# Performance work log

Hardware: AMD Instinct MI355X
Metric: run time of the kernel (lower is better)

The kernel has to match this reference:

```python
import jax, jax.numpy as jnp
import numpy as np

N, E = 50000, 1600000
IN_C, HEADS, OUT_C = 128, 4, 32


def setup_inputs() -> dict:
    key = jax.random.key(0)
    ks = jax.random.split(key, 8)
    x = jax.random.normal(ks[0], (N, IN_C), dtype=jnp.float32)
    row = jnp.sort(jax.random.randint(ks[1], (E,), 0, N, dtype=jnp.int32)).astype(jnp.int64)
    col = jax.random.randint(ks[2], (E,), 0, N, dtype=jnp.int64)
    # xavier_uniform-style params
    def xavier(k, shape, fan_in, fan_out):
        lim = float(np.sqrt(6.0 / (fan_in + fan_out)))
        return jax.random.uniform(k, shape, jnp.float32, -lim, lim)
    weight = xavier(ks[3], (IN_C, HEADS * OUT_C), IN_C, HEADS * OUT_C)
    att_src = xavier(ks[4], (1, HEADS, OUT_C), HEADS, OUT_C)
    att_dst = xavier(ks[5], (1, HEADS, OUT_C), HEADS, OUT_C)
    bias = jnp.zeros((HEADS * OUT_C,), jnp.float32)
    return {"x": x, "weight": weight, "att_src": att_src, "att_dst": att_dst,
            "bias": bias, "row": row, "col": col}


def reference(x, weight, att_src, att_dst, bias, row, col):
    n = x.shape[0]
    H, C = att_src.shape[1], att_src.shape[2]
    xp = (x @ weight).reshape(n, H, C)                 # [N,H,C]
    a_src = jnp.sum(xp * att_src, axis=-1)             # [N,H]
    a_dst = jnp.sum(xp * att_dst, axis=-1)             # [N,H]
    alpha = jax.nn.leaky_relu(a_src[row] + a_dst[col], negative_slope=0.2)  # [E,H]
    # torch scatter_reduce amax with include_self=True over a zeros buffer -> max(0, seg_max)
    amax = jnp.maximum(jax.ops.segment_max(alpha, row, num_segments=n), 0.0)
    alpha = jnp.exp(alpha - amax[row])
    asum = jax.ops.segment_sum(alpha, row, num_segments=n)
    alpha = alpha / (asum[row] + 1e-8)                 # [E,H]
    msg = alpha[:, :, None] * xp[col]                  # [E,H,C]
    out = jax.ops.segment_sum(msg, row, num_segments=n).reshape(n, H * C)
    return out + bias
```

## Files before the change

kernel.cpp:

```cpp
#include <hip/hip_runtime.h>
#include <hip/hip_bf16.h>


#define IN_C 128
#define HC 128
#define STG 256

typedef __attribute__((ext_vector_type(8))) __bf16 bfrag_t;
typedef __attribute__((ext_vector_type(4))) float f32x4;
union frag_u { uint4 u; bfrag_t b; };

static __device__ inline unsigned short f2bf(float f) {
    unsigned u = __float_as_uint(f);
    unsigned r = (u + 0x7fffu + ((u >> 16) & 1u)) >> 16;
    return (unsigned short)r;
}
static __device__ inline unsigned pack2(float a, float b) {
    return (unsigned)f2bf(a) | ((unsigned)f2bf(b) << 16);
}
static __device__ inline float bf_lo(unsigned u) { return __uint_as_float(u << 16); }
static __device__ inline float bf_hi(unsigned u) { return __uint_as_float(u & 0xffff0000u); }

__global__ __launch_bounds__(256) void prep_kernel(const float* __restrict__ W,
                                                   unsigned short* __restrict__ wt,
                                                   const int* __restrict__ row,
                                                   int* __restrict__ row_ptr,
                                                   int n_nodes, int E) {
    int gid = blockIdx.x * 256 + threadIdx.x;
    if (gid < IN_C * HC) {
        int n = gid >> 7, k = gid & 127;
        wt[((size_t)n * 16 + ((k >> 3) ^ (n & 7))) * 8 + (k & 7)] =
            f2bf(W[(size_t)k * HC + n]);
    }
    if (gid < E) {
        int lane = threadIdx.x & 63;
        int r1 = row[gid];
        int r0 = __shfl_up(r1, 1, 64);
        if (lane == 0) r0 = (gid == 0) ? -1 : row[gid - 1];
        for (int v = r0 + 1; v <= r1; ++v) row_ptr[v] = gid;
        if (gid == E - 1)
            for (int v = r1 + 1; v <= n_nodes; ++v) row_ptr[v] = E;
    }
}

__global__ __launch_bounds__(512) void gemm_kernel(const float* __restrict__ x,
                                                   const uint4* __restrict__ wt,
                                                   const float* __restrict__ attS,
                                                   const float* __restrict__ attD,
                                                   unsigned short* __restrict__ xp,
                                                   float* __restrict__ a_src,
                                                   float* __restrict__ a_dst, int n_nodes) {
    __shared__ uint4 Bl[2048];
    __shared__ uint4 Al[2048];
    const int tid = threadIdx.x;
    const int base = blockIdx.x * 128;

    #pragma unroll
    for (int i = 0; i < 4; ++i) Bl[tid + 512 * i] = wt[tid + 512 * i];

    #pragma unroll
    for (int i = 0; i < 4; ++i) {
        int idx = tid + 512 * i;
        int row = idx >> 4, chunk = idx & 15;
        uint4 p = make_uint4(0u, 0u, 0u, 0u);
        if (base + row < n_nodes) {
            const float* src = x + (size_t)(base + row) * IN_C + chunk * 8;
            float4 lo = *(const float4*)src;
            float4 hi = *(const float4*)(src + 4);
            p.x = pack2(lo.x, lo.y); p.y = pack2(lo.z, lo.w);
            p.z = pack2(hi.x, hi.y); p.w = pack2(hi.z, hi.w);
        }
        Al[row * 16 + (chunk ^ (row & 7))] = p;
    }
    __syncthreads();

    const int w = tid >> 6, l = tid & 63, l15 = l & 15, q = l >> 4;
    f32x4 acc[8] = {};
    const int arow = 16 * w + l15;
    #pragma unroll
    for (int ks = 0; ks < 4; ++ks) {
        frag_u a; a.u = Al[arow * 16 + ((ks * 4 + q) ^ (arow & 7))];
        #pragma unroll
        for (int t = 0; t < 8; ++t) {
            int brow = 16 * t + l15;
            frag_u b; b.u = Bl[brow * 16 + ((ks * 4 + q) ^ (brow & 7))];
            acc[t] = __builtin_amdgcn_mfma_f32_16x16x32_bf16(a.b, b.b, acc[t], 0, 0, 0);
        }
    }

    float avS[8], avD[8];
    #pragma unroll
    for (int t = 0; t < 8; ++t) {
        avS[t] = attS[16 * t + l15];
        avD[t] = attD[16 * t + l15];
    }
    float hpS[4][4] = {}, hpD[4][4] = {};
    #pragma unroll
    for (int t = 0; t < 8; ++t) {
        #pragma unroll
        for (int r = 0; r < 4; ++r) {
            float v = acc[t][r];
            hpS[r][t >> 1] = fmaf(v, avS[t], hpS[r][t >> 1]);
            hpD[r][t >> 1] = fmaf(v, avD[t], hpD[r][t >> 1]);
            int grow = base + 16 * w + 4 * q + r;
            if (grow < n_nodes)
                xp[(size_t)grow * HC + 16 * t + l15] = f2bf(v);
        }
    }
    #pragma unroll
    for (int r = 0; r < 4; ++r) {
        #pragma unroll
        for (int h = 0; h < 4; ++h) {
            #pragma unroll
            for (int off = 1; off < 16; off <<= 1) {
                hpS[r][h] += __shfl_xor(hpS[r][h], off, 64);
                hpD[r][h] += __shfl_xor(hpD[r][h], off, 64);
            }
        }
        int grow = base + 16 * w + 4 * q + r;
        if (l15 == 0 && grow < n_nodes) {
            *(float4*)(a_src + (size_t)grow * 4) =
                make_float4(hpS[r][0], hpS[r][1], hpS[r][2], hpS[r][3]);
            *(float4*)(a_dst + (size_t)grow * 4) =
                make_float4(hpD[r][0], hpD[r][1], hpD[r][2], hpD[r][3]);
        }
    }
}

__global__ __launch_bounds__(256, 8) void agg_kernel(const unsigned* __restrict__ xp,
                                                     const float* __restrict__ a_src,
                                                     const float* __restrict__ a_dst,
                                                     const int* __restrict__ col,
                                                     const int* __restrict__ row_ptr,
                                                     const float* __restrict__ bias,
                                                     float* __restrict__ out, int n_nodes) {
    __shared__ uint2 lds_w[4][STG];
    __shared__ int   lds_c[4][STG];
    const int wid = threadIdx.x >> 6, lane = threadIdx.x & 63;
    const int n = blockIdx.x * 4 + wid;
    const bool alive = n < n_nodes;

    int start = 0, deg = 0;
    if (alive) { start = row_ptr[n]; deg = row_ptr[n + 1] - start; }
    const bool staged = deg <= STG;
    float4 as4 = alive ? *(const float4*)(a_src + (size_t)n * 4)
                       : make_float4(0.f, 0.f, 0.f, 0.f);

    float s0 = 0.f, s1 = 0.f, s2 = 0.f, s3 = 0.f;
    for (int i = lane; i < deg; i += 64) {
        int cc = col[start + i];
        float4 ad = *(const float4*)(a_dst + (size_t)cc * 4);
        float v0 = as4.x + ad.x, v1 = as4.y + ad.y, v2 = as4.z + ad.z, v3 = as4.w + ad.w;
        v0 = v0 > 0.f ? v0 : 0.2f * v0;  v1 = v1 > 0.f ? v1 : 0.2f * v1;
        v2 = v2 > 0.f ? v2 : 0.2f * v2;  v3 = v3 > 0.f ? v3 : 0.2f * v3;
        float w0 = __expf(v0), w1 = __expf(v1), w2 = __expf(v2), w3 = __expf(v3);
        if (staged) {
            lds_c[wid][i] = cc;
            lds_w[wid][i] = make_uint2(pack2(w0, w1), pack2(w2, w3));
        }
        s0 += w0; s1 += w1; s2 += w2; s3 += w3;
    }
    #pragma unroll
    for (int off = 1; off < 64; off <<= 1) {
        s0 += __shfl_xor(s0, off, 64);
        s1 += __shfl_xor(s1, off, 64);
        s2 += __shfl_xor(s2, off, 64);
        s3 += __shfl_xor(s3, off, 64);
    }

    const int h = lane >> 4;
    const float sh = h == 0 ? s0 : h == 1 ? s1 : h == 2 ? s2 : s3;
    const float inv = 1.0f / (sh + 1e-8f);
    const unsigned* xpl = xp + lane;
    float ac0 = 0.f, ac1 = 0.f;

    if (staged) {
        const uint2* wr = &lds_w[wid][0];
        const int*   cr = &lds_c[wid][0];
        int i = 0;
        for (; i + 8 <= deg; i += 8) {
            int c0 = cr[i+0], c1 = cr[i+1], c2 = cr[i+2], c3 = cr[i+3];
            int c4 = cr[i+4], c5 = cr[i+5], c6 = cr[i+6], c7 = cr[i+7];
            uint2 q0 = wr[i+0], q1 = wr[i+1], q2 = wr[i+2], q3 = wr[i+3];
            uint2 q4 = wr[i+4], q5 = wr[i+5], q6 = wr[i+6], q7 = wr[i+7];
            unsigned u0 = xpl[(size_t)c0 * 64];
            unsigned u1 = xpl[(size_t)c1 * 64];
            unsigned u2 = xpl[(size_t)c2 * 64];
            unsigned u3 = xpl[(size_t)c3 * 64];
            unsigned u4 = xpl[(size_t)c4 * 64];
            unsigned u5 = xpl[(size_t)c5 * 64];
            unsigned u6 = xpl[(size_t)c6 * 64];
            unsigned u7 = xpl[(size_t)c7 * 64];
            unsigned x0 = (h & 2) ? q0.y : q0.x;
            unsigned x1 = (h & 2) ? q1.y : q1.x;
            unsigned x2 = (h & 2) ? q2.y : q2.x;
            unsigned x3 = (h & 2) ? q3.y : q3.x;
            unsigned x4 = (h & 2) ? q4.y : q4.x;
            unsigned x5 = (h & 2) ? q5.y : q5.x;
            unsigned x6 = (h & 2) ? q6.y : q6.x;
            unsigned x7 = (h & 2) ? q7.y : q7.x;
            float w0 = (h & 1) ? bf_hi(x0) : bf_lo(x0);
            float w1 = (h & 1) ? bf_hi(x1) : bf_lo(x1);
            float w2 = (h & 1) ? bf_hi(x2) : bf_lo(x2);
            float w3 = (h & 1) ? bf_hi(x3) : bf_lo(x3);
            float w4 = (h & 1) ? bf_hi(x4) : bf_lo(x4);
            float w5 = (h & 1) ? bf_hi(x5) : bf_lo(x5);
            float w6 = (h & 1) ? bf_hi(x6) : bf_lo(x6);
            float w7 = (h & 1) ? bf_hi(x7) : bf_lo(x7);
            ac0 = fmaf(w0, bf_lo(u0), ac0);  ac1 = fmaf(w0, bf_hi(u0), ac1);
            ac0 = fmaf(w1, bf_lo(u1), ac0);  ac1 = fmaf(w1, bf_hi(u1), ac1);
            ac0 = fmaf(w2, bf_lo(u2), ac0);  ac1 = fmaf(w2, bf_hi(u2), ac1);
            ac0 = fmaf(w3, bf_lo(u3), ac0);  ac1 = fmaf(w3, bf_hi(u3), ac1);
            ac0 = fmaf(w4, bf_lo(u4), ac0);  ac1 = fmaf(w4, bf_hi(u4), ac1);
            ac0 = fmaf(w5, bf_lo(u5), ac0);  ac1 = fmaf(w5, bf_hi(u5), ac1);
            ac0 = fmaf(w6, bf_lo(u6), ac0);  ac1 = fmaf(w6, bf_hi(u6), ac1);
            ac0 = fmaf(w7, bf_lo(u7), ac0);  ac1 = fmaf(w7, bf_hi(u7), ac1);
        }
        for (; i < deg; ++i) {
            int c0 = cr[i];
            uint2 q0 = wr[i];
            unsigned x0 = (h & 2) ? q0.y : q0.x;
            float w0 = (h & 1) ? bf_hi(x0) : bf_lo(x0);
            unsigned u0 = xpl[(size_t)c0 * 64];
            ac0 = fmaf(w0, bf_lo(u0), ac0);  ac1 = fmaf(w0, bf_hi(u0), ac1);
        }
    } else {
        const float ash = h == 0 ? as4.x : h == 1 ? as4.y : h == 2 ? as4.z : as4.w;
        for (int i = 0; i < deg; ++i) {
            int c0 = col[start + i];
            float v = ash + a_dst[(size_t)c0 * 4 + h];
            v = v > 0.f ? v : 0.2f * v;
            float w0 = __expf(v);
            unsigned u0 = xpl[(size_t)c0 * 64];
            ac0 = fmaf(w0, bf_lo(u0), ac0);  ac1 = fmaf(w0, bf_hi(u0), ac1);
        }
    }

    if (alive) {
        float2 bv = *(const float2*)(bias + 2 * lane);
        *(float2*)(out + (size_t)n * HC + 2 * lane) =
            make_float2(ac0 * inv + bv.x, ac1 * inv + bv.y);
    }
}

extern "C" void kernel_launch(void* const* d_in, const int* in_sizes, int n_in,
                              void* d_out, int out_size, void* d_ws, size_t ws_size,
                              hipStream_t stream) {
    const float* x       = (const float*)d_in[0];
    const float* weight  = (const float*)d_in[1];
    const float* att_src = (const float*)d_in[2];
    const float* att_dst = (const float*)d_in[3];
    const float* bias    = (const float*)d_in[4];
    const int*   row     = (const int*)d_in[5];
    const int*   col     = (const int*)d_in[6];
    float* out = (float*)d_out;

    const int n_nodes = in_sizes[0] / IN_C;
    const int E = in_sizes[5];

    char* ws = (char*)d_ws;
    unsigned short* xp = (unsigned short*)ws;  ws += (size_t)n_nodes * HC * sizeof(unsigned short);
    float* a_src   = (float*)ws;               ws += (size_t)n_nodes * 4 * sizeof(float);
    float* a_dst   = (float*)ws;               ws += (size_t)n_nodes * 4 * sizeof(float);
    unsigned short* wt = (unsigned short*)ws;  ws += (size_t)IN_C * HC * sizeof(unsigned short);
    int*   row_ptr = (int*)ws;                 ws += (size_t)(n_nodes + 1) * sizeof(int);

    prep_kernel<<<(E + 255) / 256, 256, 0, stream>>>(weight, wt, row, row_ptr, n_nodes, E);
    gemm_kernel<<<(n_nodes + 127) / 128, 512, 0, stream>>>(x, (const uint4*)wt,
                                                           att_src, att_dst,
                                                           xp, a_src, a_dst, n_nodes);
    agg_kernel<<<(n_nodes + 3) / 4, 256, 0, stream>>>((const unsigned*)xp, a_src, a_dst,
                                                      col, row_ptr, bias, out, n_nodes);
}
```

Before: 84.32 us.

## Move row_ptr construction into GEMM kernel and stage xp stores through LDS

The CSR row_ptr build moves out of the prep kernel, which now only converts weights with a small grid, and into the GEMM kernel, where each block handles a contiguous slice of edges. The GEMM's bf16 output is first written to shared memory and then stored to global memory as coalesced 16-byte rows, replacing scattered 2-byte stores. This is meant to shorten the large prep launch and improve write coalescing. The cost is extra LDS traffic and barriers in the GEMM, and the GEMM blocks now also do the edge scan.

```diff
diff --git a/kernel.cpp b/kernel.cpp
--- a/kernel.cpp
+++ b/kernel.cpp
@@ -22,55 +22,58 @@
 static __device__ inline float bf_hi(unsigned u) { return __uint_as_float(u & 0xffff0000u); }
 
 __global__ __launch_bounds__(256) void prep_kernel(const float* __restrict__ W,
-                                                   unsigned short* __restrict__ wt,
-                                                   const int* __restrict__ row,
-                                                   int* __restrict__ row_ptr,
-                                                   int n_nodes, int E) {
+                                                   unsigned short* __restrict__ wt) {
     int gid = blockIdx.x * 256 + threadIdx.x;
-    if (gid < IN_C * HC) {
-        int n = gid >> 7, k = gid & 127;
-        wt[((size_t)n * 16 + ((k >> 3) ^ (n & 7))) * 8 + (k & 7)] =
-            f2bf(W[(size_t)k * HC + n]);
-    }
-    if (gid < E) {
-        int lane = threadIdx.x & 63;
-        int r1 = row[gid];
-        int r0 = __shfl_up(r1, 1, 64);
-        if (lane == 0) r0 = (gid == 0) ? -1 : row[gid - 1];
-        for (int v = r0 + 1; v <= r1; ++v) row_ptr[v] = gid;
-        if (gid == E - 1)
-            for (int v = r1 + 1; v <= n_nodes; ++v) row_ptr[v] = E;
-    }
+    int n = gid >> 7, k = gid & 127;
+    wt[((size_t)n * 16 + ((k >> 3) ^ (n & 7))) * 8 + (k & 7)] =
+        f2bf(W[(size_t)k * HC + n]);
 }
 
 __global__ __launch_bounds__(512) void gemm_kernel(const float* __restrict__ x,
                                                    const uint4* __restrict__ wt,
                                                    const float* __restrict__ attS,
                                                    const float* __restrict__ attD,
+                                                   const int* __restrict__ row,
+                                                   int* __restrict__ row_ptr,
                                                    unsigned short* __restrict__ xp,
                                                    float* __restrict__ a_src,
-                                                   float* __restrict__ a_dst, int n_nodes) {
+                                                   float* __restrict__ a_dst,
+                                                   int n_nodes, int E) {
     __shared__ uint4 Bl[2048];
     __shared__ uint4 Al[2048];
     const int tid = threadIdx.x;
     const int base = blockIdx.x * 128;
 
+    {
+        const int nblk = gridDim.x;
+        const int per = (E + nblk - 1) / nblk;
+        const int e0 = blockIdx.x * per;
+        const int e1 = min(e0 + per, E);
+        for (int e = e0 + tid; e < e1; e += 512) {
+            int r1 = row[e];
+            int r0 = (e == 0) ? -1 : row[e - 1];
+            for (int v = r0 + 1; v <= r1; ++v) row_ptr[v] = e;
+            if (e == E - 1)
+                for (int v = r1 + 1; v <= n_nodes; ++v) row_ptr[v] = E;
+        }
+    }
+
     #pragma unroll
     for (int i = 0; i < 4; ++i) Bl[tid + 512 * i] = wt[tid + 512 * i];
 
     #pragma unroll
     for (int i = 0; i < 4; ++i) {
         int idx = tid + 512 * i;
-        int row = idx >> 4, chunk = idx & 15;
+        int r = idx >> 4, chunk = idx & 15;
         uint4 p = make_uint4(0u, 0u, 0u, 0u);
-        if (base + row < n_nodes) {
-            const float* src = x + (size_t)(base + row) * IN_C + chunk * 8;
+        if (base + r < n_nodes) {
+            const float* src = x + (size_t)(base + r) * IN_C + chunk * 8;
             float4 lo = *(const float4*)src;
             float4 hi = *(const float4*)(src + 4);
             p.x = pack2(lo.x, lo.y); p.y = pack2(lo.z, lo.w);
             p.z = pack2(hi.x, hi.y); p.w = pack2(hi.z, hi.w);
         }
-        Al[row * 16 + (chunk ^ (row & 7))] = p;
+        Al[r * 16 + (chunk ^ (r & 7))] = p;
     }
     __syncthreads();
 
@@ -102,9 +105,6 @@
             float v = acc[t][r];
             hpS[r][t >> 1] = fmaf(v, avS[t], hpS[r][t >> 1]);
             hpD[r][t >> 1] = fmaf(v, avD[t], hpD[r][t >> 1]);
-            int grow = base + 16 * w + 4 * q + r;
-            if (grow < n_nodes)
-                xp[(size_t)grow * HC + 16 * t + l15] = f2bf(v);
         }
     }
     #pragma unroll
@@ -124,6 +124,24 @@
             *(float4*)(a_dst + (size_t)grow * 4) =
                 make_float4(hpD[r][0], hpD[r][1], hpD[r][2], hpD[r][3]);
         }
+    }
+
+    __syncthreads();
+    unsigned short* Cl = (unsigned short*)Bl;
+    #pragma unroll
+    for (int t = 0; t < 8; ++t) {
+        #pragma unroll
+        for (int r = 0; r < 4; ++r)
+            Cl[(16 * w + 4 * q + r) * HC + 16 * t + l15] = f2bf(acc[t][r]);
+    }
+    __syncthreads();
+    const uint4* Cv = (const uint4*)Cl;
+    #pragma unroll
+    for (int i = 0; i < 4; ++i) {
+        int idx = tid + 512 * i;
+        int r = idx >> 4;
+        if (base + r < n_nodes)
+            *(uint4*)(xp + (size_t)(base + r) * HC + (idx & 15) * 8) = Cv[idx];
     }
 }
 
@@ -265,10 +283,10 @@
     unsigned short* wt = (unsigned short*)ws;  ws += (size_t)IN_C * HC * sizeof(unsigned short);
     int*   row_ptr = (int*)ws;                 ws += (size_t)(n_nodes + 1) * sizeof(int);
 
-    prep_kernel<<<(E + 255) / 256, 256, 0, stream>>>(weight, wt, row, row_ptr, n_nodes, E);
+    prep_kernel<<<64, 256, 0, stream>>>(weight, wt);
     gemm_kernel<<<(n_nodes + 127) / 128, 512, 0, stream>>>(x, (const uint4*)wt,
-                                                           att_src, att_dst,
-                                                           xp, a_src, a_dst, n_nodes);
+                                                           att_src, att_dst, row, row_ptr,
+                                                           xp, a_src, a_dst, n_nodes, E);
     agg_kernel<<<(n_nodes + 3) / 4, 256, 0, stream>>>((const unsigned*)xp, a_src, a_dst,
                                                       col, row_ptr, bias, out, n_nodes);
 }
```

After: 87.37 us. +3.6%, slower.

## Drop LDS staging in projection GEMM, load MFMA fragments directly from global

Applied to the files above, without the earlier changes.

The GEMM kernel now reads A fragments straight from global x (converting to bf16 in registers) and B fragments straight from the pre-transposed weight buffer. The shared-memory staging, XOR swizzle and barrier are removed. Blocks shrink to 256 threads covering 64 rows, which should raise occupancy. The weight matrix is now re-read from global/L2 by every wave, and the A loads are strided per lane, trading LDS traffic and sync for more cache traffic.

```diff
diff --git a/kernel.cpp b/kernel.cpp
--- a/kernel.cpp
+++ b/kernel.cpp
@@ -29,8 +29,7 @@
     int gid = blockIdx.x * 256 + threadIdx.x;
     if (gid < IN_C * HC) {
         int n = gid >> 7, k = gid & 127;
-        wt[((size_t)n * 16 + ((k >> 3) ^ (n & 7))) * 8 + (k & 7)] =
-            f2bf(W[(size_t)k * HC + n]);
+        wt[((size_t)n * 16 + (k >> 3)) * 8 + (k & 7)] = f2bf(W[(size_t)k * HC + n]);
     }
     if (gid < E) {
         int lane = threadIdx.x & 63;
@@ -43,47 +42,35 @@
     }
 }
 
-__global__ __launch_bounds__(512) void gemm_kernel(const float* __restrict__ x,
-                                                   const uint4* __restrict__ wt,
+__global__ __launch_bounds__(256) void gemm_kernel(const float* __restrict__ x,
+                                                   const uint4* __restrict__ wtv,
                                                    const float* __restrict__ attS,
                                                    const float* __restrict__ attD,
                                                    unsigned short* __restrict__ xp,
                                                    float* __restrict__ a_src,
                                                    float* __restrict__ a_dst, int n_nodes) {
-    __shared__ uint4 Bl[2048];
-    __shared__ uint4 Al[2048];
     const int tid = threadIdx.x;
-    const int base = blockIdx.x * 128;
-
-    #pragma unroll
-    for (int i = 0; i < 4; ++i) Bl[tid + 512 * i] = wt[tid + 512 * i];
-
-    #pragma unroll
-    for (int i = 0; i < 4; ++i) {
-        int idx = tid + 512 * i;
-        int row = idx >> 4, chunk = idx & 15;
-        uint4 p = make_uint4(0u, 0u, 0u, 0u);
-        if (base + row < n_nodes) {
-            const float* src = x + (size_t)(base + row) * IN_C + chunk * 8;
-            float4 lo = *(const float4*)src;
-            float4 hi = *(const float4*)(src + 4);
-            p.x = pack2(lo.x, lo.y); p.y = pack2(lo.z, lo.w);
-            p.z = pack2(hi.x, hi.y); p.w = pack2(hi.z, hi.w);
-        }
-        Al[row * 16 + (chunk ^ (row & 7))] = p;
-    }
-    __syncthreads();
-
+    const int base = blockIdx.x * 64;
     const int w = tid >> 6, l = tid & 63, l15 = l & 15, q = l >> 4;
+    const int arow = base + 16 * w + l15;
+    const bool arok = arow < n_nodes;
+    const float* ap = x + (size_t)(arok ? arow : 0) * IN_C + 8 * q;
+
     f32x4 acc[8] = {};
-    const int arow = 16 * w + l15;
     #pragma unroll
     for (int ks = 0; ks < 4; ++ks) {
-        frag_u a; a.u = Al[arow * 16 + ((ks * 4 + q) ^ (arow & 7))];
+        frag_u a;
+        if (arok) {
+            float4 lo = *(const float4*)(ap + ks * 32);
+            float4 hi = *(const float4*)(ap + ks * 32 + 4);
+            a.u.x = pack2(lo.x, lo.y); a.u.y = pack2(lo.z, lo.w);
+            a.u.z = pack2(hi.x, hi.y); a.u.w = pack2(hi.z, hi.w);
+        } else {
+            a.u = make_uint4(0u, 0u, 0u, 0u);
+        }
         #pragma unroll
         for (int t = 0; t < 8; ++t) {
-            int brow = 16 * t + l15;
-            frag_u b; b.u = Bl[brow * 16 + ((ks * 4 + q) ^ (brow & 7))];
+            frag_u b; b.u = wtv[(16 * t + l15) * 16 + ks * 4 + q];
             acc[t] = __builtin_amdgcn_mfma_f32_16x16x32_bf16(a.b, b.b, acc[t], 0, 0, 0);
         }
     }
@@ -266,9 +253,9 @@
     int*   row_ptr = (int*)ws;                 ws += (size_t)(n_nodes + 1) * sizeof(int);
 
     prep_kernel<<<(E + 255) / 256, 256, 0, stream>>>(weight, wt, row, row_ptr, n_nodes, E);
-    gemm_kernel<<<(n_nodes + 127) / 128, 512, 0, stream>>>(x, (const uint4*)wt,
-                                                           att_src, att_dst,
-                                                           xp, a_src, a_dst, n_nodes);
+    gemm_kernel<<<(n_nodes + 63) / 64, 256, 0, stream>>>(x, (const uint4*)wt,
+                                                         att_src, att_dst,
+                                                         xp, a_src, a_dst, n_nodes);
     agg_kernel<<<(n_nodes + 3) / 4, 256, 0, stream>>>((const unsigned*)xp, a_src, a_dst,
                                                       col, row_ptr, bias, out, n_nodes);
 }
```

Result: slower. 94.90 us (+12.5%).
